# Performance work log

Measured on AMD Instinct MI355X. Metric: run time of the kernel, lower is better.

## Reference

```python
import jax, jax.numpy as jnp
import numpy as np

INF = 1e10  # sentinel 'infinity' for non-feature pixels (safe to add (s*N)^2 without overflow)


def _edt_sq_last(f, s):
    """Exact 1D squared distance transform along the last axis.
    f: (..., N) initialized to 0 at feature pixels, INF elsewhere.
    Returns g[..., i] = min_j f[..., j] + (s*(i-j))^2.
    Sequential lax.scan over output positions keeps memory at O(N) extra."""
    N = f.shape[-1]
    j = jnp.arange(N, dtype=f.dtype)

    def step(_, i):
        return None, jnp.min(f + (s * (i - j)) ** 2, axis=-1)

    _, out = jax.lax.scan(step, None, jnp.arange(N, dtype=f.dtype))
    return jnp.moveaxis(out, 0, -1)


def _edt(feature_mask, sampling):
    """Euclidean distance to the nearest True pixel of feature_mask (2D, anisotropic sampling).
    Equivalent to scipy.ndimage.distance_transform_edt(~feature_mask, sampling=sampling)."""
    f = jnp.where(feature_mask, 0.0, INF).astype(jnp.float32)
    # pass over axis -2 (rows), then axis -1 (cols) -- exact separable squared EDT
    f = jnp.moveaxis(_edt_sq_last(jnp.moveaxis(f, -2, -1), sampling[0]), -1, -2)
    f = _edt_sq_last(f, sampling[1])
    return jnp.sqrt(f)


def _distance_map(y_onehot, sampling):
    """res = edt_to_pos * negmask - (edt_to_neg - 1) * posmask, 0 where class absent."""
    pos = y_onehot              # (B,K,H,W) bool
    neg = ~pos
    d_neg = _edt(pos, sampling)  # distance of neg pixels to nearest pos pixel
    d_pos = _edt(neg, sampling)  # distance of pos pixels to nearest neg pixel
    res = jnp.where(neg, d_neg, 0.0) - jnp.where(pos, d_pos - 1.0, 0.0)
    has_pos = pos.any(axis=(-2, -1), keepdims=True)  # scipy path leaves res[k]=0 if class absent
    return jnp.where(has_pos, res, 0.0)


def reference(x, y):
    # x: (B,K,H,W) float; y: (B,1,H,W) int labels in [0,K)
    K = x.shape[1]
    y_onehot = (y == jnp.arange(K, dtype=y.dtype)[None, :, None, None])  # scatter_ onehot
    dist_map = jax.lax.stop_gradient(_distance_map(y_onehot, (1.0, 1.0)))
    return jnp.mean(x * dist_map)  # einsum('bkwh,bkwh->bkwh').mean()


def setup_inputs() -> dict:
    key = jax.random.key(0)
    k1, k2 = jax.random.split(key)
    x = jax.random.normal(k1, (8, 4, 256, 256), dtype=jnp.float32)
    y = jax.random.randint(k2, (8, 1, 256, 256), 0, 4, dtype=jnp.int32)
    return {"x": x, "y": y}
```

## Files before the change

kernel.cpp:

```cpp
#include <hip/hip_runtime.h>


#define HH 256
#define WW 256
#define NPIX (HH*WW)
#define NPM 64
#define BIG (1 << 27)
#define NSTRIPE 64

#define SEGS 8
#define RSEG 32
#define CPB 32

__global__ void edt_vpass(const int* __restrict__ y, unsigned short* __restrict__ g,
                          double* __restrict__ acc, unsigned int* __restrict__ cnt) {
    __shared__ unsigned short d[HH][CPB + 1];
    __shared__ short segLast[SEGS][CPB];
    __shared__ short segFirst[SEGS][CPB];

    int bid   = blockIdx.x;
    int pm    = bid >> 3;
    int cc    = bid & 7;
    int which = pm & 1;
    int plane = pm >> 1;
    int b     = plane >> 2;
    int k     = plane & 3;

    int t   = threadIdx.x;
    int col = t & (CPB - 1);
    int seg = t >> 5;
    int w   = cc * CPB + col;
    int h0  = seg * RSEG;

    if (bid == 0) {
        acc[t] = 0.0; acc[t + 256] = 0.0;
        if (t == 0) *cnt = 0u;
    }

    const int* yp = y + b * NPIX;
    unsigned short* gp = g + (size_t)pm * NPIX;

    int lastL = -1000, firstL = 1000;
    for (int i = 0; i < RSEG; ++i) {
        int h   = h0 + i;
        int lab = yp[h * WW + w];
        int feat = ((lab == k) ? 1 : 0) ^ which;
        if (feat) { lastL = h; if (firstL > 900) firstL = h; }
        d[h][col] = (unsigned short)min(h - lastL, 1000);
    }
    segLast[seg][col]  = (short)lastL;
    segFirst[seg][col] = (short)firstL;
    __syncthreads();

    int prevLast = -1000;
    for (int s = seg - 1; s >= 0; --s) {
        int v = segLast[s][col];
        if (v >= 0) { prevLast = v; break; }
    }
    int nextFirst = 1000;
    for (int s = seg + 1; s < SEGS; ++s) {
        int v = segFirst[s][col];
        if (v < 900) { nextFirst = v; break; }
    }

    int nd = nextFirst;
    for (int i = RSEG - 1; i >= 0; --i) {
        int h  = h0 + i;
        int du = d[h][col];
        if (du == 0) nd = h;
        int dup = min(du, h - prevLast);
        int ddn = nd - h;
        int m   = min(min(dup, ddn), 256);
        gp[h * WW + w] = (m > 255) ? (unsigned short)0xFFFF
                                   : (unsigned short)(m * m);
    }
}

#define ROWS_PER_BLK 16
#define NBLK2 1024

__global__ void edt_hpass(const unsigned short* __restrict__ g,
                          const float* __restrict__ x,
                          double* __restrict__ acc, unsigned int* __restrict__ cnt,
                          float* __restrict__ out) {
    __shared__ int tile[ROWS_PER_BLK][WW];
    __shared__ double wsum[4];
    __shared__ int lastFlag;

    int bid   = blockIdx.x;
    int pm    = bid >> 4;
    int rc    = bid & 15;
    int r0    = rc * ROWS_PER_BLK;
    int which = pm & 1;
    int plane = pm >> 1;
    int t     = threadIdx.x;

    const unsigned short* gp = g + (size_t)pm * NPIX;
    const float* xp = x + (size_t)plane * NPIX;

    const unsigned int* gp32 = (const unsigned int*)(gp + r0 * WW);
    for (int i2 = 0; i2 < 8; ++i2) {
        int idx = i2 * 256 + t;
        int row = idx >> 7;
        int c2  = idx & 127;
        unsigned int v = gp32[row * 128 + c2];
        int v0 = (int)(v & 0xFFFFu);
        int v1 = (int)(v >> 16);
        tile[row][2 * c2]     = (v0 == 0xFFFF) ? BIG : v0;
        tile[row][2 * c2 + 1] = (v1 == 0xFFFF) ? BIG : v1;
    }
    __syncthreads();

    double lsum = 0.0;
    for (int i = 0; i < ROWS_PER_BLK; ++i) {
        int best = tile[i][t];
        float xv = xp[(r0 + i) * WW + t];
        #pragma unroll 1
        for (int bs = 1; bs < WW; bs += 4) {
            if (bs * bs >= best) break;
            int m = best;
            #pragma unroll
            for (int u = 0; u < 4; ++u) {
                int r  = bs + u;
                int rr = r * r;
                int jl = max(t - r, 0);
                int jr = min(t + r, WW - 1);
                m = min(m, tile[i][jl] + rr);
                m = min(m, tile[i][jr] + rr);
            }
            best = m;
        }
        if (best > 0 && best < BIG) {
            float dd   = sqrtf((float)best);
            float term = which ? (1.0f - dd) : dd;
            lsum += (double)(xv * term);
        }
    }

    for (int off = 32; off > 0; off >>= 1)
        lsum += __shfl_down(lsum, off, 64);
    int lane = t & 63, wv = t >> 6;
    if (lane == 0) wsum[wv] = lsum;
    __syncthreads();

    if (t == 0) {
        double s = wsum[0] + wsum[1] + wsum[2] + wsum[3];
        atomicAdd(&acc[(bid & (NSTRIPE - 1)) * 8], s);
        asm volatile("s_waitcnt vmcnt(0)" ::: "memory");
        unsigned int ticket = atomicAdd(cnt, 1u);
        lastFlag = (ticket == NBLK2 - 1) ? 1 : 0;
    }
    __syncthreads();

    if (lastFlag && t < 64) {
        double v = atomicAdd(&acc[t * 8], 0.0);
        for (int off = 32; off > 0; off >>= 1)
            v += __shfl_down(v, off, 64);
        if (t == 0) out[0] = (float)(v * (1.0 / 2097152.0));
    }
}

extern "C" void kernel_launch(void* const* d_in, const int* in_sizes, int n_in,
                              void* d_out, int out_size, void* d_ws, size_t ws_size,
                              hipStream_t stream) {
    const float* x = (const float*)d_in[0];
    const int*   y = (const int*)d_in[1];
    float* out = (float*)d_out;

    unsigned short* g   = (unsigned short*)d_ws;
    double*         acc = (double*)((char*)d_ws + (size_t)NPM * NPIX * sizeof(unsigned short));
    unsigned int*   cnt = (unsigned int*)((char*)acc + 512 * sizeof(double));

    edt_vpass<<<512,  256, 0, stream>>>(y, g, acc, cnt);
    edt_hpass<<<NBLK2, 256, 0, stream>>>(g, x, acc, cnt, out);
}
```

Measured before the change: 83.97 us.

## Fuse vertical and horizontal EDT passes into one kernel without intermediate buffer

Merges the column pass and row pass into a single kernel. Each block scans its full column segment directly from the label array, keeps squared vertical distances in a 64-row shared tile, and then runs the horizontal min search on that tile. This removes the 16-bit intermediate global buffer and one kernel launch, and loads x only for pixels that contribute to the sum. In exchange each block rescans most of the column (redundant label reads), only 256 blocks are launched so occupancy drops, and the accumulator is now cleared with a memset.

Result: slower. 172.1 us (+105.0%).

```diff
diff --git a/kernel.cpp b/kernel.cpp
--- a/kernel.cpp
+++ b/kernel.cpp
@@ -7,114 +7,52 @@
 #define NPM 64
 #define BIG (1 << 27)
 #define NSTRIPE 64
+#define RPB 64
+#define NBLK 256
 
-#define SEGS 8
-#define RSEG 32
-#define CPB 32
-
-__global__ void edt_vpass(const int* __restrict__ y, unsigned short* __restrict__ g,
-                          double* __restrict__ acc, unsigned int* __restrict__ cnt) {
-    __shared__ unsigned short d[HH][CPB + 1];
-    __shared__ short segLast[SEGS][CPB];
-    __shared__ short segFirst[SEGS][CPB];
+__global__ void boundary_all(const int* __restrict__ y, const float* __restrict__ x,
+                             double* __restrict__ acc, unsigned int* __restrict__ cnt,
+                             float* __restrict__ out) {
+    __shared__ int tile[RPB][WW];
+    __shared__ double wsum[4];
+    __shared__ int lastFlag;
 
     int bid   = blockIdx.x;
-    int pm    = bid >> 3;
-    int cc    = bid & 7;
+    int pm    = bid >> 2;
+    int rc    = bid & 3;
+    int r0    = rc * RPB;
     int which = pm & 1;
     int plane = pm >> 1;
     int b     = plane >> 2;
     int k     = plane & 3;
-
-    int t   = threadIdx.x;
-    int col = t & (CPB - 1);
-    int seg = t >> 5;
-    int w   = cc * CPB + col;
-    int h0  = seg * RSEG;
-
-    if (bid == 0) {
-        acc[t] = 0.0; acc[t + 256] = 0.0;
-        if (t == 0) *cnt = 0u;
-    }
-
-    const int* yp = y + b * NPIX;
-    unsigned short* gp = g + (size_t)pm * NPIX;
-
-    int lastL = -1000, firstL = 1000;
-    for (int i = 0; i < RSEG; ++i) {
-        int h   = h0 + i;
-        int lab = yp[h * WW + w];
-        int feat = ((lab == k) ? 1 : 0) ^ which;
-        if (feat) { lastL = h; if (firstL > 900) firstL = h; }
-        d[h][col] = (unsigned short)min(h - lastL, 1000);
-    }
-    segLast[seg][col]  = (short)lastL;
-    segFirst[seg][col] = (short)firstL;
-    __syncthreads();
-
-    int prevLast = -1000;
-    for (int s = seg - 1; s >= 0; --s) {
-        int v = segLast[s][col];
-        if (v >= 0) { prevLast = v; break; }
-    }
-    int nextFirst = 1000;
-    for (int s = seg + 1; s < SEGS; ++s) {
-        int v = segFirst[s][col];
-        if (v < 900) { nextFirst = v; break; }
-    }
-
-    int nd = nextFirst;
-    for (int i = RSEG - 1; i >= 0; --i) {
-        int h  = h0 + i;
-        int du = d[h][col];
-        if (du == 0) nd = h;
-        int dup = min(du, h - prevLast);
-        int ddn = nd - h;
-        int m   = min(min(dup, ddn), 256);
-        gp[h * WW + w] = (m > 255) ? (unsigned short)0xFFFF
-                                   : (unsigned short)(m * m);
-    }
-}
-
-#define ROWS_PER_BLK 16
-#define NBLK2 1024
-
-__global__ void edt_hpass(const unsigned short* __restrict__ g,
-                          const float* __restrict__ x,
-                          double* __restrict__ acc, unsigned int* __restrict__ cnt,
-                          float* __restrict__ out) {
-    __shared__ int tile[ROWS_PER_BLK][WW];
-    __shared__ double wsum[4];
-    __shared__ int lastFlag;
-
-    int bid   = blockIdx.x;
-    int pm    = bid >> 4;
-    int rc    = bid & 15;
-    int r0    = rc * ROWS_PER_BLK;
-    int which = pm & 1;
-    int plane = pm >> 1;
     int t     = threadIdx.x;
 
-    const unsigned short* gp = g + (size_t)pm * NPIX;
+    const int*   yp = y + b * NPIX;
     const float* xp = x + (size_t)plane * NPIX;
 
-    const unsigned int* gp32 = (const unsigned int*)(gp + r0 * WW);
-    for (int i2 = 0; i2 < 8; ++i2) {
-        int idx = i2 * 256 + t;
-        int row = idx >> 7;
-        int c2  = idx & 127;
-        unsigned int v = gp32[row * 128 + c2];
-        int v0 = (int)(v & 0xFFFFu);
-        int v1 = (int)(v >> 16);
-        tile[row][2 * c2]     = (v0 == 0xFFFF) ? BIG : v0;
-        tile[row][2 * c2 + 1] = (v1 == 0xFFFF) ? BIG : v1;
+    int last = -1000;
+    int hEnd = r0 + RPB;
+    for (int h = 0; h < hEnd; ++h) {
+        int lab  = yp[h * WW + t];
+        int feat = ((lab == k) ? 1 : 0) ^ which;
+        if (feat) last = h;
+        if (h >= r0) tile[h - r0][t] = h - last;
+    }
+    int nxt = 1000;
+    for (int h = HH - 1; h >= r0; --h) {
+        int lab  = yp[h * WW + t];
+        int feat = ((lab == k) ? 1 : 0) ^ which;
+        if (feat) nxt = h;
+        if (h < hEnd) {
+            int m = min(min(tile[h - r0][t], nxt - h), 256);
+            tile[h - r0][t] = (m > 255) ? BIG : m * m;
+        }
     }
     __syncthreads();
 
     double lsum = 0.0;
-    for (int i = 0; i < ROWS_PER_BLK; ++i) {
+    for (int i = 0; i < RPB; ++i) {
         int best = tile[i][t];
-        float xv = xp[(r0 + i) * WW + t];
         #pragma unroll 1
         for (int bs = 1; bs < WW; bs += 4) {
             if (bs * bs >= best) break;
@@ -131,6 +69,7 @@
             best = m;
         }
         if (best > 0 && best < BIG) {
+            float xv   = xp[(r0 + i) * WW + t];
             float dd   = sqrtf((float)best);
             float term = which ? (1.0f - dd) : dd;
             lsum += (double)(xv * term);
@@ -148,7 +87,7 @@
         atomicAdd(&acc[(bid & (NSTRIPE - 1)) * 8], s);
         asm volatile("s_waitcnt vmcnt(0)" ::: "memory");
         unsigned int ticket = atomicAdd(cnt, 1u);
-        lastFlag = (ticket == NBLK2 - 1) ? 1 : 0;
+        lastFlag = (ticket == NBLK - 1) ? 1 : 0;
     }
     __syncthreads();
 
@@ -167,10 +106,9 @@
     const int*   y = (const int*)d_in[1];
     float* out = (float*)d_out;
 
-    unsigned short* g   = (unsigned short*)d_ws;
-    double*         acc = (double*)((char*)d_ws + (size_t)NPM * NPIX * sizeof(unsigned short));
-    unsigned int*   cnt = (unsigned int*)((char*)acc + 512 * sizeof(double));
+    double*       acc = (double*)d_ws;
+    unsigned int* cnt = (unsigned int*)((char*)d_ws + 4096);
 
-    edt_vpass<<<512,  256, 0, stream>>>(y, g, acc, cnt);
-    edt_hpass<<<NBLK2, 256, 0, stream>>>(g, x, acc, cnt, out);
+    hipMemsetAsync(d_ws, 0, 4104, stream);
+    boundary_all<<<NBLK, 256, 0, stream>>>(y, x, acc, cnt, out);
 }
```
